# Performance work log

Measured on AMD Instinct MI355X. Metric: run time of the kernel, lower is better.

## Reference

```python
import jax, jax.numpy as jnp
import numpy as np

B, K, N = 8, 4, 131072
T = B * K * N  # upper bound on packed length
NEG_IDLE = -1e8   # logit value forced when slot is idle
NEG_FILL = -1000.0  # padded-output fill value for logits


def setup_inputs() -> dict:
    key = jax.random.key(0)
    k1, k2, k3, k4, k5, k6 = jax.random.split(key, 6)
    return {
        "rgb": jax.random.normal(k1, (T, 3), dtype=jnp.float32),
        "logits_surface": jax.random.normal(k2, (T, 1), dtype=jnp.float32),
        "logits_air": jax.random.normal(k3, (T, 1), dtype=jnp.float32),
        "mask_surface": jax.random.bernoulli(k4, 0.5, (B, K, N)),
        "mask_air": jax.random.bernoulli(k5, 0.5, (B, K, N)),
        "idle_states": jax.random.uniform(k6, (B, K), dtype=jnp.float32),
    }


def reference(rgb, logits_surface, logits_air, mask_surface, mask_air, idle_states):
    # Packed arrays are laid out in flattened (b, k, n) order: the packed index of a
    # masked element equals the count of True entries preceding it -> cumsum - 1.
    Bb, Kk, Nn = mask_surface.shape
    scale = (1.0 - idle_states)[:, :, None, None]          # [B,K,1,1]
    idle = idle_states[:, :, None, None]                   # [B,K,1,1]

    ms_flat = mask_surface.reshape(-1)
    idx_s = (jnp.cumsum(ms_flat.astype(jnp.int32)) - 1).reshape(Bb, Kk, Nn)
    ms = mask_surface[..., None]                           # [B,K,N,1]

    rgb_g = jnp.take(rgb, idx_s, axis=0)                   # [B,K,N,3]
    rgb_out = jnp.where(ms, rgb_g * scale, 0.0)

    ls_g = jnp.take(logits_surface, idx_s, axis=0)         # [B,K,N,1]
    logits_surface_out = jnp.where(ms, ls_g * scale + idle * NEG_IDLE, NEG_FILL)

    ma_flat = mask_air.reshape(-1)
    idx_a = (jnp.cumsum(ma_flat.astype(jnp.int32)) - 1).reshape(Bb, Kk, Nn)
    ma = mask_air[..., None]
    la_g = jnp.take(logits_air, idx_a, axis=0)             # [B,K,N,1]
    logits_air_out = jnp.where(ma, la_g * scale + idle * NEG_IDLE, NEG_FILL)

    return rgb_out, logits_surface_out, logits_air_out
```

## Files before the change

### kernel.cpp

```cpp
#include <hip/hip_runtime.h>
#include <stdint.h>

#define T_TOTAL  4194304
#define NEG_IDLE (-100000000.0f)
#define NEG_FILL (-1000.0f)

#define BLOCK            256
#define ELEMS_PER_THREAD 16
#define ELEMS_PER_BLOCK  (BLOCK * ELEMS_PER_THREAD)
#define NBLOCKS          (T_TOTAL / ELEMS_PER_BLOCK)

#define WS_FLAG_OFF   0
#define WS_SUMS_OFF   16
#define WS_PACK_OFF   (16 + 2 * NBLOCKS * (int)sizeof(int))
#define WS_PACK_BYTES (NBLOCKS * BLOCK * (int)sizeof(unsigned int))
#define WS_NEEDED     ((size_t)WS_PACK_OFF + (size_t)WS_PACK_BYTES)

__device__ __forceinline__ unsigned int decode16_i32(const unsigned int* p) {
    unsigned int bits = 0;
    #pragma unroll
    for (int q = 0; q < 4; ++q) {
        uint4 v = ((const uint4*)p)[q];
        bits |= (v.x ? 1u : 0u) << (4 * q + 0);
        bits |= (v.y ? 1u : 0u) << (4 * q + 1);
        bits |= (v.z ? 1u : 0u) << (4 * q + 2);
        bits |= (v.w ? 1u : 0u) << (4 * q + 3);
    }
    return bits;
}

__device__ __forceinline__ unsigned int decode16_u8(const uint8_t* p) {
    const ulonglong2 v = *(const ulonglong2*)p;
    unsigned int bits = 0;
    #pragma unroll
    for (int j = 0; j < 8; ++j) bits |= (unsigned int)((v.x >> (8 * j)) & 1ull) << j;
    #pragma unroll
    for (int j = 0; j < 8; ++j) bits |= (unsigned int)((v.y >> (8 * j)) & 1ull) << (8 + j);
    return bits;
}

__device__ __forceinline__ unsigned int decode16(const void* m, size_t elem_base, int is_i32) {
    return is_i32 ? decode16_i32((const unsigned int*)m + elem_base)
                  : decode16_u8((const uint8_t*)m + elem_base);
}

__global__ __launch_bounds__(64) void detect_kernel(const unsigned long long* m,
                                                    int* flag) {
    const int lane = threadIdx.x;
    unsigned long long o = 0;
    #pragma unroll
    for (int q = 0; q < 8; ++q) o |= m[lane * 8 + q];
    #pragma unroll
    for (int d = 32; d > 0; d >>= 1) o |= __shfl_down(o, d, 64);
    if (lane == 0) *flag = ((o & 0xFFFFFFFEFFFFFFFEull) == 0ull) ? 1 : 0;
}

__global__ __launch_bounds__(BLOCK) void reduce_pack_kernel(
    const void* __restrict__ ms,
    const void* __restrict__ ma,
    const int* __restrict__ flag,
    int* __restrict__ sums_s,
    int* __restrict__ sums_a,
    unsigned int* __restrict__ packed,
    int have_pack)
{
    const int blk  = blockIdx.x;
    const int tid  = threadIdx.x;
    const int lane = tid & 63;
    const size_t base = (size_t)blk * ELEMS_PER_BLOCK + (size_t)tid * ELEMS_PER_THREAD;
    const int is_i32 = *flag;

    const unsigned int bits_s = decode16(ms, base, is_i32);
    const unsigned int bits_a = decode16(ma, base, is_i32);

    if (have_pack) packed[blk * BLOCK + tid] = bits_s | (bits_a << 16);

    const int cs = __popc(bits_s);
    const int ca = __popc(bits_a);

    unsigned long long v = ((unsigned long long)(unsigned)ca << 32) | (unsigned)cs;
    #pragma unroll
    for (int d = 32; d > 0; d >>= 1)
        v += __shfl_down(v, d, 64);

    __shared__ unsigned long long wsum[BLOCK / 64];
    if (lane == 0) wsum[tid >> 6] = v;
    __syncthreads();
    if (tid == 0) {
        unsigned long long t = 0;
        #pragma unroll
        for (int w = 0; w < BLOCK / 64; ++w) t += wsum[w];
        sums_s[blk] = (int)(t & 0xffffffffULL);
        sums_a[blk] = (int)(t >> 32);
    }
}

__global__ __launch_bounds__(1024) void scan_kernel(
    int* __restrict__ sums_s,
    int* __restrict__ sums_a)
{
    const int tid = threadIdx.x;
    const unsigned long long v =
        ((unsigned long long)(unsigned)sums_a[tid] << 32) | (unsigned)sums_s[tid];

    __shared__ unsigned long long tmp[NBLOCKS];
    tmp[tid] = v;
    __syncthreads();
    #pragma unroll
    for (int d = 1; d < NBLOCKS; d <<= 1) {
        unsigned long long t = (tid >= d) ? tmp[tid - d] : 0ULL;
        __syncthreads();
        tmp[tid] += t;
        __syncthreads();
    }
    const unsigned long long excl = tmp[tid] - v;
    sums_s[tid] = (int)(excl & 0xffffffffULL);
    sums_a[tid] = (int)(excl >> 32);
}

template <int MODE>
__global__ __launch_bounds__(BLOCK) void scatter_kernel(
    const float* __restrict__ rgb,
    const float* __restrict__ ls,
    const float* __restrict__ la,
    const void* __restrict__ ms,
    const void* __restrict__ ma,
    const int* __restrict__ flag,
    const unsigned int* __restrict__ packed,
    const float* __restrict__ idle_states,
    const int* __restrict__ off_s_arr,
    const int* __restrict__ off_a_arr,
    float* __restrict__ out)
{
    const int blk  = blockIdx.x;
    const int tid  = threadIdx.x;
    const int lane = tid & 63;
    const int wave = tid >> 6;
    const size_t base = (size_t)blk * ELEMS_PER_BLOCK + (size_t)tid * ELEMS_PER_THREAD;

    unsigned int bits_s, bits_a;
    if (MODE == 0) {
        const unsigned int p = packed[blk * BLOCK + tid];
        bits_s = p & 0xffffu;
        bits_a = p >> 16;
    } else {
        const int is_i32 = *flag;
        bits_s = decode16(ms, base, is_i32);
        bits_a = decode16(ma, base, is_i32);
    }

    const int cs = __popc(bits_s);
    const int ca = __popc(bits_a);

    const unsigned long long pack = ((unsigned long long)(unsigned)ca << 32) | (unsigned)cs;
    unsigned long long incl = pack;
    #pragma unroll
    for (int d = 1; d < 64; d <<= 1) {
        unsigned long long t = __shfl_up(incl, d, 64);
        if (lane >= d) incl += t;
    }
    unsigned long long excl = incl - pack;

    __shared__ unsigned long long wtot[BLOCK / 64];
    if (lane == 63) wtot[wave] = incl;
    __syncthreads();
    #pragma unroll
    for (int w = 0; w < BLOCK / 64; ++w)
        if (w < wave) excl += wtot[w];

    int idx_s = off_s_arr[blk] + (int)(excl & 0xffffffffULL);
    int idx_a = off_a_arr[blk] + (int)(excl >> 32);

    const float idle      = idle_states[blk >> 5];
    const float scale     = 1.0f - idle;
    const float idle_term = idle * NEG_IDLE;

    float orgb[3 * ELEMS_PER_THREAD];
    float ols[ELEMS_PER_THREAD];
    float ola[ELEMS_PER_THREAD];

    #pragma unroll
    for (int j = 0; j < ELEMS_PER_THREAD; ++j) {
        const bool bs = (bits_s >> j) & 1u;
        const bool ba = (bits_a >> j) & 1u;

        const float* rp = rgb + (size_t)idx_s * 3;
        const float r0 = rp[0], r1 = rp[1], r2 = rp[2];
        const float lsv = ls[idx_s];
        const float lav = la[idx_a];

        orgb[j * 3 + 0] = bs ? r0 * scale : 0.0f;
        orgb[j * 3 + 1] = bs ? r1 * scale : 0.0f;
        orgb[j * 3 + 2] = bs ? r2 * scale : 0.0f;
        ols[j] = bs ? (lsv * scale + idle_term) : NEG_FILL;
        ola[j] = ba ? (lav * scale + idle_term) : NEG_FILL;

        idx_s += bs ? 1 : 0;
        idx_a += ba ? 1 : 0;
    }

    float4* prgb = (float4*)(out + base * 3);
    #pragma unroll
    for (int j = 0; j < 12; ++j) prgb[j] = ((const float4*)orgb)[j];

    float4* pls = (float4*)(out + (size_t)3 * T_TOTAL + base);
    #pragma unroll
    for (int j = 0; j < 4; ++j) pls[j] = ((const float4*)ols)[j];

    float4* pla = (float4*)(out + (size_t)4 * T_TOTAL + base);
    #pragma unroll
    for (int j = 0; j < 4; ++j) pla[j] = ((const float4*)ola)[j];
}

extern "C" void kernel_launch(void* const* d_in, const int* in_sizes, int n_in,
                              void* d_out, int out_size, void* d_ws, size_t ws_size,
                              hipStream_t stream) {
    const float* rgb  = (const float*)d_in[0];
    const float* ls   = (const float*)d_in[1];
    const float* la   = (const float*)d_in[2];
    const void*  ms   = d_in[3];
    const void*  ma   = d_in[4];
    const float* idle = (const float*)d_in[5];
    float* out = (float*)d_out;

    uint8_t* ws = (uint8_t*)d_ws;
    int* flag   = (int*)(ws + WS_FLAG_OFF);
    int* sums_s = (int*)(ws + WS_SUMS_OFF);
    int* sums_a = sums_s + NBLOCKS;
    unsigned int* packed = (unsigned int*)(ws + WS_PACK_OFF);
    const int have_pack = (ws_size >= WS_NEEDED) ? 1 : 0;

    detect_kernel<<<1, 64, 0, stream>>>((const unsigned long long*)ms, flag);
    reduce_pack_kernel<<<NBLOCKS, BLOCK, 0, stream>>>(ms, ma, flag, sums_s, sums_a,
                                                      have_pack ? packed : nullptr,
                                                      have_pack);
    scan_kernel<<<1, NBLOCKS, 0, stream>>>(sums_s, sums_a);
    if (have_pack) {
        scatter_kernel<0><<<NBLOCKS, BLOCK, 0, stream>>>(rgb, ls, la, ms, ma, flag,
                                                         packed, idle, sums_s, sums_a, out);
    } else {
        scatter_kernel<1><<<NBLOCKS, BLOCK, 0, stream>>>(rgb, ls, la, ms, ma, flag,
                                                         packed, idle, sums_s, sums_a, out);
    }
}
```

Measured before the change: 208.5 us.

## Fuse reduce, scan and scatter into single-pass decoupled look-back kernel

Replaces the detect/reduce/scan/scatter pipeline with one kernel that computes block prefix offsets with a decoupled look-back over per-block status slots, plus a small init kernel that clears the slots. This removes the extra passes over the masks, the packed-bits round trip and three kernel launches. The mask dtype detection is dropped and masks are assumed to be int32, and output stores are now interleaved in groups of four. Correctness depends on blocks being scheduled in order, on the 24-bit packed count fields not overflowing, and on spin-waiting with atomics.

```diff
diff --git a/kernel.cpp b/kernel.cpp
--- a/kernel.cpp
+++ b/kernel.cpp
@@ -5,22 +5,23 @@
 #define NEG_IDLE (-100000000.0f)
 #define NEG_FILL (-1000.0f)
 
-#define BLOCK            256
-#define ELEMS_PER_THREAD 16
-#define ELEMS_PER_BLOCK  (BLOCK * ELEMS_PER_THREAD)
-#define NBLOCKS          (T_TOTAL / ELEMS_PER_BLOCK)
+#define BLOCK   256
+#define EPT     16
+#define EPB     (BLOCK * EPT)
+#define NBLOCKS (T_TOTAL / EPB)
 
-#define WS_FLAG_OFF   0
-#define WS_SUMS_OFF   16
-#define WS_PACK_OFF   (16 + 2 * NBLOCKS * (int)sizeof(int))
-#define WS_PACK_BYTES (NBLOCKS * BLOCK * (int)sizeof(unsigned int))
-#define WS_NEEDED     ((size_t)WS_PACK_OFF + (size_t)WS_PACK_BYTES)
+#define ST_AGG 1ull
+#define ST_PRE 2ull
 
-__device__ __forceinline__ unsigned int decode16_i32(const unsigned int* p) {
+__device__ __forceinline__ uint64_t pack_counts(uint32_t cs, uint32_t ca) {
+    return ((uint64_t)cs << 2) | ((uint64_t)ca << 26);
+}
+
+__device__ __forceinline__ unsigned int decode16_i32(const uint4* p) {
     unsigned int bits = 0;
     #pragma unroll
     for (int q = 0; q < 4; ++q) {
-        uint4 v = ((const uint4*)p)[q];
+        const uint4 v = p[q];
         bits |= (v.x ? 1u : 0u) << (4 * q + 0);
         bits |= (v.y ? 1u : 0u) << (4 * q + 1);
         bits |= (v.z ? 1u : 0u) << (4 * q + 2);
@@ -29,187 +30,133 @@
     return bits;
 }
 
-__device__ __forceinline__ unsigned int decode16_u8(const uint8_t* p) {
-    const ulonglong2 v = *(const ulonglong2*)p;
-    unsigned int bits = 0;
-    #pragma unroll
-    for (int j = 0; j < 8; ++j) bits |= (unsigned int)((v.x >> (8 * j)) & 1ull) << j;
-    #pragma unroll
-    for (int j = 0; j < 8; ++j) bits |= (unsigned int)((v.y >> (8 * j)) & 1ull) << (8 + j);
-    return bits;
+__global__ __launch_bounds__(BLOCK) void init_kernel(unsigned long long* slots) {
+    const int i = blockIdx.x * BLOCK + threadIdx.x;
+    if (i < NBLOCKS) slots[i] = 0ull;
 }
 
-__device__ __forceinline__ unsigned int decode16(const void* m, size_t elem_base, int is_i32) {
-    return is_i32 ? decode16_i32((const unsigned int*)m + elem_base)
-                  : decode16_u8((const uint8_t*)m + elem_base);
-}
-
-__global__ __launch_bounds__(64) void detect_kernel(const unsigned long long* m,
-                                                    int* flag) {
-    const int lane = threadIdx.x;
-    unsigned long long o = 0;
-    #pragma unroll
-    for (int q = 0; q < 8; ++q) o |= m[lane * 8 + q];
-    #pragma unroll
-    for (int d = 32; d > 0; d >>= 1) o |= __shfl_down(o, d, 64);
-    if (lane == 0) *flag = ((o & 0xFFFFFFFEFFFFFFFEull) == 0ull) ? 1 : 0;
-}
-
-__global__ __launch_bounds__(BLOCK) void reduce_pack_kernel(
-    const void* __restrict__ ms,
-    const void* __restrict__ ma,
-    const int* __restrict__ flag,
-    int* __restrict__ sums_s,
-    int* __restrict__ sums_a,
-    unsigned int* __restrict__ packed,
-    int have_pack)
-{
-    const int blk  = blockIdx.x;
-    const int tid  = threadIdx.x;
-    const int lane = tid & 63;
-    const size_t base = (size_t)blk * ELEMS_PER_BLOCK + (size_t)tid * ELEMS_PER_THREAD;
-    const int is_i32 = *flag;
-
-    const unsigned int bits_s = decode16(ms, base, is_i32);
-    const unsigned int bits_a = decode16(ma, base, is_i32);
-
-    if (have_pack) packed[blk * BLOCK + tid] = bits_s | (bits_a << 16);
-
-    const int cs = __popc(bits_s);
-    const int ca = __popc(bits_a);
-
-    unsigned long long v = ((unsigned long long)(unsigned)ca << 32) | (unsigned)cs;
-    #pragma unroll
-    for (int d = 32; d > 0; d >>= 1)
-        v += __shfl_down(v, d, 64);
-
-    __shared__ unsigned long long wsum[BLOCK / 64];
-    if (lane == 0) wsum[tid >> 6] = v;
-    __syncthreads();
-    if (tid == 0) {
-        unsigned long long t = 0;
-        #pragma unroll
-        for (int w = 0; w < BLOCK / 64; ++w) t += wsum[w];
-        sums_s[blk] = (int)(t & 0xffffffffULL);
-        sums_a[blk] = (int)(t >> 32);
-    }
-}
-
-__global__ __launch_bounds__(1024) void scan_kernel(
-    int* __restrict__ sums_s,
-    int* __restrict__ sums_a)
-{
-    const int tid = threadIdx.x;
-    const unsigned long long v =
-        ((unsigned long long)(unsigned)sums_a[tid] << 32) | (unsigned)sums_s[tid];
-
-    __shared__ unsigned long long tmp[NBLOCKS];
-    tmp[tid] = v;
-    __syncthreads();
-    #pragma unroll
-    for (int d = 1; d < NBLOCKS; d <<= 1) {
-        unsigned long long t = (tid >= d) ? tmp[tid - d] : 0ULL;
-        __syncthreads();
-        tmp[tid] += t;
-        __syncthreads();
-    }
-    const unsigned long long excl = tmp[tid] - v;
-    sums_s[tid] = (int)(excl & 0xffffffffULL);
-    sums_a[tid] = (int)(excl >> 32);
-}
-
-template <int MODE>
-__global__ __launch_bounds__(BLOCK) void scatter_kernel(
+__global__ __launch_bounds__(BLOCK, 6) void fused_kernel(
     const float* __restrict__ rgb,
     const float* __restrict__ ls,
     const float* __restrict__ la,
-    const void* __restrict__ ms,
-    const void* __restrict__ ma,
-    const int* __restrict__ flag,
-    const unsigned int* __restrict__ packed,
+    const uint4* __restrict__ ms,
+    const uint4* __restrict__ ma,
     const float* __restrict__ idle_states,
-    const int* __restrict__ off_s_arr,
-    const int* __restrict__ off_a_arr,
+    unsigned long long* __restrict__ slots,
     float* __restrict__ out)
 {
     const int blk  = blockIdx.x;
     const int tid  = threadIdx.x;
     const int lane = tid & 63;
     const int wave = tid >> 6;
-    const size_t base = (size_t)blk * ELEMS_PER_BLOCK + (size_t)tid * ELEMS_PER_THREAD;
+    const size_t base = (size_t)blk * EPB + (size_t)tid * EPT;
 
-    unsigned int bits_s, bits_a;
-    if (MODE == 0) {
-        const unsigned int p = packed[blk * BLOCK + tid];
-        bits_s = p & 0xffffu;
-        bits_a = p >> 16;
-    } else {
-        const int is_i32 = *flag;
-        bits_s = decode16(ms, base, is_i32);
-        bits_a = decode16(ma, base, is_i32);
-    }
-
+    const unsigned int bits_s = decode16_i32(ms + (base >> 2));
+    const unsigned int bits_a = decode16_i32(ma + (base >> 2));
     const int cs = __popc(bits_s);
     const int ca = __popc(bits_a);
 
-    const unsigned long long pack = ((unsigned long long)(unsigned)ca << 32) | (unsigned)cs;
-    unsigned long long incl = pack;
+    const unsigned long long pk = ((unsigned long long)(unsigned)ca << 32) | (unsigned)cs;
+    unsigned long long incl = pk;
     #pragma unroll
     for (int d = 1; d < 64; d <<= 1) {
         unsigned long long t = __shfl_up(incl, d, 64);
         if (lane >= d) incl += t;
     }
-    unsigned long long excl = incl - pack;
+    unsigned long long excl = incl - pk;
 
     __shared__ unsigned long long wtot[BLOCK / 64];
+    __shared__ unsigned long long sPre;
     if (lane == 63) wtot[wave] = incl;
     __syncthreads();
     #pragma unroll
     for (int w = 0; w < BLOCK / 64; ++w)
         if (w < wave) excl += wtot[w];
 
-    int idx_s = off_s_arr[blk] + (int)(excl & 0xffffffffULL);
-    int idx_a = off_a_arr[blk] + (int)(excl >> 32);
+    const unsigned long long tot = wtot[0] + wtot[1] + wtot[2] + wtot[3];
+    const uint64_t aggpack = pack_counts((uint32_t)tot, (uint32_t)(tot >> 32));
+
+    if (tid == 0) {
+        const uint64_t val = aggpack | ((blk == 0) ? ST_PRE : ST_AGG);
+        __hip_atomic_store(&slots[blk], val, __ATOMIC_RELEASE, __HIP_MEMORY_SCOPE_AGENT);
+        if (blk == 0) sPre = 0ull;
+    }
+    if (blk != 0 && wave == 0) {
+        int look = blk - 1;
+        uint64_t acc = 0;
+        for (;;) {
+            const int src = look - lane;
+            uint64_t v;
+            for (;;) {
+                v = (src >= 0)
+                    ? __hip_atomic_load(&slots[src], __ATOMIC_ACQUIRE, __HIP_MEMORY_SCOPE_AGENT)
+                    : ST_PRE;
+                if (__all((v & 3ull) != 0ull)) break;
+                __builtin_amdgcn_s_sleep(1);
+            }
+            const unsigned long long pm = __ballot((v & 3ull) == ST_PRE);
+            uint64_t contrib = v & ~3ull;
+            int L = -1;
+            if (pm) {
+                L = __ffsll((long long)pm) - 1;
+                if (lane > L) contrib = 0;
+            }
+            uint64_t s = contrib;
+            #pragma unroll
+            for (int d = 32; d; d >>= 1) s += __shfl_down(s, d, 64);
+            acc += __shfl(s, 0, 64);
+            if (pm) break;
+            look -= 64;
+        }
+        if (lane == 0) {
+            sPre = acc;
+            __hip_atomic_store(&slots[blk], (acc + aggpack) | ST_PRE,
+                               __ATOMIC_RELEASE, __HIP_MEMORY_SCOPE_AGENT);
+        }
+    }
+    __syncthreads();
+
+    const uint64_t pre = sPre;
+    int idx_s = (int)((pre >> 2)  & 0xFFFFFFull) + (int)(excl & 0xffffffffULL);
+    int idx_a = (int)((pre >> 26) & 0xFFFFFFull) + (int)(excl >> 32);
 
     const float idle      = idle_states[blk >> 5];
     const float scale     = 1.0f - idle;
     const float idle_term = idle * NEG_IDLE;
 
-    float orgb[3 * ELEMS_PER_THREAD];
-    float ols[ELEMS_PER_THREAD];
-    float ola[ELEMS_PER_THREAD];
+    float4* prgb = (float4*)(out + base * 3);
+    float4* pls  = (float4*)(out + (size_t)3 * T_TOTAL + base);
+    float4* pla  = (float4*)(out + (size_t)4 * T_TOTAL + base);
 
     #pragma unroll
-    for (int j = 0; j < ELEMS_PER_THREAD; ++j) {
-        const bool bs = (bits_s >> j) & 1u;
-        const bool ba = (bits_a >> j) & 1u;
+    for (int g = 0; g < 4; ++g) {
+        float og[12], sg[4], ag[4];
+        #pragma unroll
+        for (int jj = 0; jj < 4; ++jj) {
+            const int j = g * 4 + jj;
+            const bool bs = (bits_s >> j) & 1u;
+            const bool ba = (bits_a >> j) & 1u;
 
-        const float* rp = rgb + (size_t)idx_s * 3;
-        const float r0 = rp[0], r1 = rp[1], r2 = rp[2];
-        const float lsv = ls[idx_s];
-        const float lav = la[idx_a];
+            const float* rp = rgb + (size_t)idx_s * 3;
+            const float r0 = rp[0], r1 = rp[1], r2 = rp[2];
+            const float lsv = ls[idx_s];
+            const float lav = la[idx_a];
 
-        orgb[j * 3 + 0] = bs ? r0 * scale : 0.0f;
-        orgb[j * 3 + 1] = bs ? r1 * scale : 0.0f;
-        orgb[j * 3 + 2] = bs ? r2 * scale : 0.0f;
-        ols[j] = bs ? (lsv * scale + idle_term) : NEG_FILL;
-        ola[j] = ba ? (lav * scale + idle_term) : NEG_FILL;
+            og[jj * 3 + 0] = bs ? r0 * scale : 0.0f;
+            og[jj * 3 + 1] = bs ? r1 * scale : 0.0f;
+            og[jj * 3 + 2] = bs ? r2 * scale : 0.0f;
+            sg[jj] = bs ? (lsv * scale + idle_term) : NEG_FILL;
+            ag[jj] = ba ? (lav * scale + idle_term) : NEG_FILL;
 
-        idx_s += bs ? 1 : 0;
-        idx_a += ba ? 1 : 0;
+            idx_s += bs ? 1 : 0;
+            idx_a += ba ? 1 : 0;
+        }
+        prgb[g * 3 + 0] = ((const float4*)og)[0];
+        prgb[g * 3 + 1] = ((const float4*)og)[1];
+        prgb[g * 3 + 2] = ((const float4*)og)[2];
+        pls[g] = ((const float4*)sg)[0];
+        pla[g] = ((const float4*)ag)[0];
     }
-
-    float4* prgb = (float4*)(out + base * 3);
-    #pragma unroll
-    for (int j = 0; j < 12; ++j) prgb[j] = ((const float4*)orgb)[j];
-
-    float4* pls = (float4*)(out + (size_t)3 * T_TOTAL + base);
-    #pragma unroll
-    for (int j = 0; j < 4; ++j) pls[j] = ((const float4*)ols)[j];
-
-    float4* pla = (float4*)(out + (size_t)4 * T_TOTAL + base);
-    #pragma unroll
-    for (int j = 0; j < 4; ++j) pla[j] = ((const float4*)ola)[j];
 }
 
 extern "C" void kernel_launch(void* const* d_in, const int* in_sizes, int n_in,
@@ -218,28 +165,14 @@
     const float* rgb  = (const float*)d_in[0];
     const float* ls   = (const float*)d_in[1];
     const float* la   = (const float*)d_in[2];
-    const void*  ms   = d_in[3];
-    const void*  ma   = d_in[4];
+    const uint4* ms   = (const uint4*)d_in[3];
+    const uint4* ma   = (const uint4*)d_in[4];
     const float* idle = (const float*)d_in[5];
     float* out = (float*)d_out;
 
-    uint8_t* ws = (uint8_t*)d_ws;
-    int* flag   = (int*)(ws + WS_FLAG_OFF);
-    int* sums_s = (int*)(ws + WS_SUMS_OFF);
-    int* sums_a = sums_s + NBLOCKS;
-    unsigned int* packed = (unsigned int*)(ws + WS_PACK_OFF);
-    const int have_pack = (ws_size >= WS_NEEDED) ? 1 : 0;
+    unsigned long long* slots = (unsigned long long*)d_ws;
 
-    detect_kernel<<<1, 64, 0, stream>>>((const unsigned long long*)ms, flag);
-    reduce_pack_kernel<<<NBLOCKS, BLOCK, 0, stream>>>(ms, ma, flag, sums_s, sums_a,
-                                                      have_pack ? packed : nullptr,
-                                                      have_pack);
-    scan_kernel<<<1, NBLOCKS, 0, stream>>>(sums_s, sums_a);
-    if (have_pack) {
-        scatter_kernel<0><<<NBLOCKS, BLOCK, 0, stream>>>(rgb, ls, la, ms, ma, flag,
-                                                         packed, idle, sums_s, sums_a, out);
-    } else {
-        scatter_kernel<1><<<NBLOCKS, BLOCK, 0, stream>>>(rgb, ls, la, ms, ma, flag,
-                                                         packed, idle, sums_s, sums_a, out);
-    }
+    init_kernel<<<(NBLOCKS + BLOCK - 1) / BLOCK, BLOCK, 0, stream>>>(slots);
+    fused_kernel<<<NBLOCKS, BLOCK, 0, stream>>>(rgb, ls, la, ms, ma, idle,
+                                                slots, out);
 }
```

Result: slower. 349.0 us (+67.4%).
